# Performance work log

Hardware: AMD Instinct MI355X
Metric: run time of the kernel (lower is better)

Reference implementation:

```python
import jax, jax.numpy as jnp
import numpy as np

N_EMBD = 1024
N_HEAD = 16
HEAD_DIM = N_EMBD // N_HEAD

def setup_inputs() -> dict:
    key = jax.random.key(0)
    ks = jax.random.split(key, 5)
    B, T, C = 2, 2048, N_EMBD
    s = 1.0 / np.sqrt(C)
    x = jax.random.normal(ks[0], (B, T, C), dtype=jnp.float32)
    W_qkv = jax.random.normal(ks[1], (C, 3 * C), dtype=jnp.float32) * s
    b_qkv = jax.random.normal(ks[2], (3 * C,), dtype=jnp.float32) * 0.02
    W_o = jax.random.normal(ks[3], (C, C), dtype=jnp.float32) * s
    b_o = jax.random.normal(ks[4], (C,), dtype=jnp.float32) * 0.02
    return {"x": x, "W_qkv": W_qkv, "b_qkv": b_qkv, "W_o": W_o, "b_o": b_o}

def reference(x, W_qkv, b_qkv, W_o, b_o):
    B, T, C = x.shape
    H, D = N_HEAD, HEAD_DIM
    scale = 1.0 / np.sqrt(D)
    qkv = jnp.einsum('btc,cf->btf', x, W_qkv) + b_qkv  # [B,T,3C]
    q, k, v = jnp.split(qkv, 3, axis=-1)
    # [B,H,T,D]
    q = q.reshape(B, T, H, D).transpose(0, 2, 1, 3)
    k = k.reshape(B, T, H, D).transpose(0, 2, 1, 3)
    v = v.reshape(B, T, H, D).transpose(0, 2, 1, 3)
    att = jnp.einsum('bhqd,bhkd->bhqk', q, k) * scale  # [B,H,T,T]
    causal = jnp.tril(jnp.ones((T, T), dtype=bool))
    att = jnp.where(causal[None, None], att, -jnp.inf)
    att = jax.nn.softmax(att, axis=-1)
    y = jnp.einsum('bhqk,bhkd->bhqd', att, v)  # [B,H,T,D]
    y = y.transpose(0, 2, 1, 3).reshape(B, T, C)
    return jnp.einsum('btc,cf->btf', y, W_o) + b_o
```

## Files before the change

### kernel.cpp

```cpp
#include <hip/hip_runtime.h>
#include <hip/hip_bf16.h>

#define TT 2048
#define BB 2
#define CC 1024
#define NH 16
#define HD 64

typedef __attribute__((ext_vector_type(8))) short short8;
typedef __attribute__((ext_vector_type(4))) short short4b;
typedef __attribute__((ext_vector_type(4))) float f32x4;

typedef unsigned int __attribute__((address_space(1))) ui_gas;
typedef unsigned int __attribute__((address_space(3))) ui_las;

#if __has_builtin(__builtin_amdgcn_mfma_f32_16x16x16bf16_1k)
#define PV16 1
#define VSS 4
#else
#define PV16 0
#define VSS 8
#endif

__device__ __forceinline__ float us2f(unsigned short u) {
    union { unsigned int i; float f; } v; v.i = ((unsigned int)u) << 16; return v.f;
}
__device__ __forceinline__ unsigned short f2us(float f) {
    union { float f; unsigned int i; } v; v.f = f;
    unsigned int i = v.i;
    unsigned int lsb = (i >> 16) & 1u;
    i += 0x7fffu + lsb;
    return (unsigned short)(i >> 16);
}
__device__ __forceinline__ unsigned int pack2_trunc(float a, float b) {
    union { float f; unsigned int u; } x, y; x.f = a; y.f = b;
    return (y.u & 0xffff0000u) | (x.u >> 16);
}

__device__ __forceinline__ void gl_lds16(const unsigned short* g, unsigned short* l) {
    __builtin_amdgcn_global_load_lds((const ui_gas*)g, (ui_las*)l, 16, 0, 0);
}

__device__ __forceinline__ float4 load4(const void* p, size_t i, int isbf) {
    if (isbf) {
        ushort4 u = *reinterpret_cast<const ushort4*>((const unsigned short*)p + i);
        return make_float4(us2f(u.x), us2f(u.y), us2f(u.z), us2f(u.w));
    } else {
        return *reinterpret_cast<const float4*>((const float*)p + i);
    }
}
__device__ __forceinline__ float load1(const void* p, size_t i, int isbf) {
    return isbf ? us2f(((const unsigned short*)p)[i]) : ((const float*)p)[i];
}

__global__ __launch_bounds__(256) void prep_kernel(
    const void* __restrict__ x, const void* __restrict__ Wqkv, const void* __restrict__ Wo,
    const void* __restrict__ bqkv, const void* __restrict__ bo,
    unsigned short* __restrict__ xb, unsigned short* __restrict__ Wqkvt,
    unsigned short* __restrict__ Wot, int* __restrict__ flags)
{
    __shared__ float Ls[64 * 65];
    __shared__ int sh_isbf;
    const int t = threadIdx.x;
    const int bid = blockIdx.x;

    const void* src;
    int mode, sub;
    if (bid < 2048)      { mode = 0; sub = bid;        src = x; }
    else if (bid < 2816) { mode = 1; sub = bid - 2048; src = Wqkv; }
    else                 { mode = 2; sub = bid - 2816; src = Wo; }

    if (bid == 0 && t < 64) {
        const void* ps[5] = {x, Wqkv, bqkv, Wo, bo};
        for (int k = 0; k < 5; ++k) {
            const unsigned short* u = (const unsigned short*)ps[k];
            int bad = 0;
            #pragma unroll
            for (int j = 0; j < 4; ++j) {
                float v = us2f(u[t * 4 + j]);
                if (!(fabsf(v) < 1e4f)) bad = 1;
            }
            unsigned long long m = __ballot(bad != 0);
            if (t == 0) flags[k] = (__popcll(m) < 4) ? 1 : 0;
        }
    }
    if (t < 64) {
        const unsigned short* u = (const unsigned short*)src;
        int bad = 0;
        #pragma unroll
        for (int j = 0; j < 4; ++j) {
            float v = us2f(u[t * 4 + j]);
            if (!(fabsf(v) < 1e4f)) bad = 1;
        }
        unsigned long long m = __ballot(bad != 0);
        if (t == 0) sh_isbf = (__popcll(m) < 4) ? 1 : 0;
    }
    __syncthreads();
    const int isbf = sh_isbf;

    if (mode == 0) {
        const size_t i = ((size_t)sub * 256 + t) * 8;
        float4 a = load4(src, i, isbf);
        float4 b = load4(src, i + 4, isbf);
        alignas(16) unsigned short pk[8];
        pk[0] = f2us(a.x); pk[1] = f2us(a.y); pk[2] = f2us(a.z); pk[3] = f2us(a.w);
        pk[4] = f2us(b.x); pk[5] = f2us(b.y); pk[6] = f2us(b.z); pk[7] = f2us(b.w);
        *reinterpret_cast<uint4*>(xb + i) = *reinterpret_cast<const uint4*>(pk);
        return;
    }

    int N, Krows, n0, k0;
    unsigned short* dst;
    if (mode == 1) { N = 3 * CC; Krows = CC; dst = Wqkvt; n0 = (sub % 48) * 64; k0 = (sub / 48) * 64; }
    else           { N = CC;     Krows = CC; dst = Wot;   n0 = (sub % 16) * 64; k0 = (sub / 16) * 64; }
    {
        const int r = t >> 2, cq = (t & 3) << 4;
        #pragma unroll
        for (int i = 0; i < 4; ++i) {
            float4 v = load4(src, (size_t)(k0 + r) * N + n0 + cq + i * 4, isbf);
            Ls[r * 65 + cq + i * 4 + 0] = v.x;
            Ls[r * 65 + cq + i * 4 + 1] = v.y;
            Ls[r * 65 + cq + i * 4 + 2] = v.z;
            Ls[r * 65 + cq + i * 4 + 3] = v.w;
        }
    }
    __syncthreads();
    {
        const int c = t & 63, kg = (t >> 6) * 16;
        alignas(16) unsigned short pk[16];
        #pragma unroll
        for (int i = 0; i < 16; ++i) pk[i] = f2us(Ls[(kg + i) * 65 + c]);
        unsigned short* d = dst + (size_t)(n0 + c) * Krows + k0 + kg;
        *reinterpret_cast<uint4*>(d + 0) = *reinterpret_cast<const uint4*>(&pk[0]);
        *reinterpret_cast<uint4*>(d + 8) = *reinterpret_cast<const uint4*>(&pk[8]);
    }
}

template<int WM, int WN, int NWM, int NWN, int SWZ, bool VTE>
__global__ __launch_bounds__(256) void gemm_mfma(
    const unsigned short* __restrict__ A,
    const unsigned short* __restrict__ Bt,
    const void* __restrict__ bias, void* __restrict__ C,
    unsigned short* __restrict__ Vt,
    int M, int N, int K,
    const int* __restrict__ flags, int biasfi, int cfi)
{
    constexpr int BM = WM * 16 * NWM, BN = WN * 16 * NWN;
    constexpr int ASL = BM / 16, BSL = BN / 16;
    constexpr int TOT = ASL + BSL;
    constexpr int PW  = TOT / 4;

    __shared__ __align__(16) unsigned short SH[3][TOT * 512];

    const int tid = threadIdx.x;
    const int l  = tid & 63;
    const int w  = tid >> 6;
    const int wm = w / NWN, wn = w % NWN;
    const int lm = l & 15;
    const int lk = (l >> 4) * 8;
    const int quad = l >> 4;

    int bx, by;
    if constexpr (SWZ == 1) {
        const int lin = blockIdx.y * 24 + blockIdx.x;
        const int xcd = lin & 7, loc = lin >> 3;
        bx = (xcd & 1) * 12 + loc % 12;
        by = (xcd >> 1) * 8 + loc / 12;
    } else if constexpr (SWZ == 2) {
        const int lin = blockIdx.y * 16 + blockIdx.x;
        const int xcd = lin & 7, loc = lin >> 3;
        bx = (xcd & 1) * 8 + (loc & 7);
        by = (xcd >> 1) * 16 + (loc >> 3);
    } else {
        bx = blockIdx.x; by = blockIdx.y;
    }
    const int bm = by * BM, bn = bx * BN;

    f32x4 acc[WM][WN];
    #pragma unroll
    for (int i = 0; i < WM; ++i)
        #pragma unroll
        for (int j = 0; j < WN; ++j) acc[i][j] = (f32x4){0.f, 0.f, 0.f, 0.f};

    auto stage = [&](int bb, int k0) {
        #pragma unroll
        for (int s = 0; s < PW; ++s) {
            const int slab = w * PW + s;
            const unsigned short* src;
            if (slab < ASL) src = A  + (size_t)(bm + slab * 16 + lm) * K + k0 + lk;
            else            src = Bt + (size_t)(bn + (slab - ASL) * 16 + lm) * K + k0 + lk;
            gl_lds16(src, &SH[bb][slab * 512]);
        }
    };

    auto compute = [&](int bb) {
        short8 af[WM], bf[WN];
        #pragma unroll
        for (int i = 0; i < WM; ++i)
            af[i] = *reinterpret_cast<const short8*>(&SH[bb][(wm * WM + i) * 512 + l * 8]);
        #pragma unroll
        for (int j = 0; j < WN; ++j)
            bf[j] = *reinterpret_cast<const short8*>(&SH[bb][(ASL + wn * WN + j) * 512 + l * 8]);
        #pragma unroll
        for (int i = 0; i < WM; ++i)
            #pragma unroll
            for (int j = 0; j < WN; ++j)
                acc[i][j] = __builtin_amdgcn_mfma_f32_16x16x32_bf16(af[i], bf[j], acc[i][j], 0, 0, 0);
    };

    const int nt = K >> 5;
    stage(0, 0);
    stage(1, 32);
    asm volatile("s_waitcnt vmcnt(%0)" :: "n"(PW) : "memory");
    __builtin_amdgcn_sched_barrier(0);
    __builtin_amdgcn_s_barrier();

    for (int t = 0; t < nt; ++t) {
        if (t + 2 < nt) stage((t + 2) % 3, (t + 2) << 5);
        compute(t % 3);
        if (t + 2 < nt) {
            asm volatile("s_waitcnt vmcnt(%0)" :: "n"(PW) : "memory");
        } else {
            asm volatile("s_waitcnt vmcnt(0)" ::: "memory");
        }
        __builtin_amdgcn_sched_barrier(0);
        __builtin_amdgcn_s_barrier();
    }

    const int bias_bf = (biasfi >= 0) ? flags[biasfi] : 0;
    const int c_bf    = (cfi >= 0) ? flags[cfi] : ((cfi == -2) ? 1 : 0);
    float bv[WN];
    #pragma unroll
    for (int j = 0; j < WN; ++j) bv[j] = load1(bias, bn + (WN * wn + j) * 16 + lm, bias_bf);

    constexpr int TS = BM + 8;
    unsigned short* FL = &SH[0][0];
    const bool vblk = VTE && (bn >= 2 * CC);

    #pragma unroll
    for (int i = 0; i < WM; ++i) {
        #pragma unroll
        for (int r = 0; r < 4; ++r) {
            const int rl = (WM * wm + i) * 16 + quad * 4 + r;
            const int row = bm + rl;
            #pragma unroll
            for (int j = 0; j < WN; ++j) {
                const int cl2 = (WN * wn + j) * 16 + lm;
                const int col = bn + cl2;
                const float val = acc[i][j][r] + bv[j];
                if (c_bf) {
                    const unsigned short us = f2us(val);
                    ((unsigned short*)C)[(size_t)row * N + col] = us;
                    if (vblk) FL[cl2 * TS + rl] = us;
                } else {
                    ((float*)C)[(size_t)row * N + col] = val;
                }
            }
        }
    }

    if constexpr (VTE) {
        static_assert(!VTE || (BM == 128 && BN % 64 == 0), "VTE geometry");
        static_assert(!VTE || (BN * (BM + 8) <= 3 * TOT * 512), "VTE LDS overlay");
        if (vblk) {
            __syncthreads();
            const int cl = tid >> 1, rq = tid & 1;
            const int cc2 = bn - 2 * CC + cl;
            const int hh = cc2 >> 6, dd = cc2 & 63;
            const int bq = bm >> 11;
            const int tk = (bm & (TT - 1)) + rq * 64;
            unsigned short* dst = Vt + ((size_t)(bq * NH + hh) * HD + dd) * TT + tk;
            const unsigned short* srcp = &FL[cl * TS + rq * 64];
            #pragma unroll
            for (int k = 0; k < 8; ++k)
                *(uint4*)(dst + k * 8) = *(const uint4*)(srcp + k * 8);
        }
    }
}

__global__ __launch_bounds__(256) void attn_mfma(
    const unsigned short* __restrict__ qkv,
    const unsigned short* __restrict__ Vt,
    unsigned short* __restrict__ y)
{
    __shared__ __align__(16) unsigned short Ksh[2][8 * 512];
    __shared__ __align__(16) unsigned short Vsh[2][1039 * VSS];

    const int tid = threadIdx.x;
    const int l   = tid & 63;
    const int w   = tid >> 6;
    const int quad = l >> 4;
    const int col  = l & 15;

    const int n  = blockIdx.x;
    const int g  = n >> 3;
    const int bh = (n & 7) * 4 + (g & 3);
    const int i  = g >> 2;
    const int tA = i, tB = 31 - i;
    const int b  = bh >> 4, h = bh & 15;

#if !PV16
    {
        unsigned short* vflat = &Vsh[0][0];
        for (int ss = tid; ss < 1039 * 2; ss += 256)
            *(uint2*)(&vflat[ss * 8 + 4]) = make_uint2(0u, 0u);
    }
#endif

    const float QSCALE = 0.18033688f;
    short8 qfA[2], qfB[2];
    #pragma unroll
    for (int t2 = 0; t2 < 2; ++t2) {
        const int qt = t2 ? tB : tA;
        short8* qf = t2 ? qfB : qfA;
        const int token = qt * 64 + w * 16 + col;
        const unsigned short* qrow = qkv + (size_t)(b * TT + token) * 3 * CC + h * HD;
        #pragma unroll
        for (int ks = 0; ks < 2; ++ks) {
            ushort4 u0 = *(const ushort4*)(qrow + ks * 32 + quad * 8);
            ushort4 u1 = *(const ushort4*)(qrow + ks * 32 + quad * 8 + 4);
            alignas(16) unsigned short pk[8];
            pk[0] = f2us(us2f(u0.x) * QSCALE);
            pk[1] = f2us(us2f(u0.y) * QSCALE);
            pk[2] = f2us(us2f(u0.z) * QSCALE);
            pk[3] = f2us(us2f(u0.w) * QSCALE);
            pk[4] = f2us(us2f(u1.x) * QSCALE);
            pk[5] = f2us(us2f(u1.y) * QSCALE);
            pk[6] = f2us(us2f(u1.z) * QSCALE);
            pk[7] = f2us(us2f(u1.w) * QSCALE);
            qf[ks] = *(const short8*)pk;
        }
    }

    f32x4 oA[4], oB[4];
    #pragma unroll
    for (int nb = 0; nb < 4; ++nb) {
        oA[nb] = (f32x4){0.f, 0.f, 0.f, 0.f};
        oB[nb] = (f32x4){0.f, 0.f, 0.f, 0.f};
    }
    float lAc = 0.f, lBc = 0.f;

    const unsigned short* kbase = qkv + (size_t)b * TT * 3 * CC + CC + h * HD;
    const unsigned short* vbase = Vt + (size_t)bh * HD * TT;

    const int vd = tid >> 2, vg0 = (tid & 3) * 4;

    uint4 rk[2], rv[2];
    auto issue_loads = [&](int kt) {
        const unsigned short* ksrc = kbase + (size_t)(kt * 64 + l) * 3 * CC;
        #pragma unroll
        for (int c2 = 0; c2 < 2; ++c2) {
            const int c = 2 * w + c2;
            rk[c2] = *(const uint4*)(ksrc + c * 8);
        }
        const unsigned short* vsrc = vbase + (size_t)vd * TT + kt * 64 + vg0 * 4;
        rv[0] = *(const uint4*)(vsrc + 0);
        rv[1] = *(const uint4*)(vsrc + 8);
    };
    auto write_lds = [&](int bb) {
        #pragma unroll
        for (int c2 = 0; c2 < 2; ++c2) {
            const int c = 2 * w + c2;
            const int ks = c >> 2, q = c & 3;
            const int slot = ((quad * 2 + ks) * 64 + q * 16 + col) * 8;
            *(uint4*)(&Ksh[bb][slot]) = rk[c2];
        }
        *(uint2*)(&Vsh[bb][((vg0 + 0) * 65 + vd) * VSS]) = make_uint2(rv[0].x, rv[0].y);
        *(uint2*)(&Vsh[bb][((vg0 + 1) * 65 + vd) * VSS]) = make_uint2(rv[0].z, rv[0].w);
        *(uint2*)(&Vsh[bb][((vg0 + 2) * 65 + vd) * VSS]) = make_uint2(rv[1].x, rv[1].y);
        *(uint2*)(&Vsh[bb][((vg0 + 3) * 65 + vd) * VSS]) = make_uint2(rv[1].z, rv[1].w);
    };

    auto step = [&](const short8* qf, f32x4* o, float& l_i, bool diag, int bb) {
        f32x4 st[4];
        __builtin_amdgcn_s_setprio(1);
        #pragma unroll
        for (int nb = 0; nb < 4; ++nb) {
            f32x4 acc = {0.f, 0.f, 0.f, 0.f};
            #pragma unroll
            for (int ks = 0; ks < 2; ++ks) {
                short8 kf = *(const short8*)(&Ksh[bb][((nb * 2 + ks) * 64 + l) * 8]);
                acc = __builtin_amdgcn_mfma_f32_16x16x32_bf16(kf, qf[ks], acc, 0, 0, 0);
            }
            st[nb] = acc;
        }
        __builtin_amdgcn_s_setprio(0);
        float pv[4][4];
        float rs = 0.f;
        #pragma unroll
        for (int nb = 0; nb < 4; ++nb)
            #pragma unroll
            for (int r = 0; r < 4; ++r) {
                float v = st[nb][r];
                if (diag && (nb * 16 + quad * 4 + r > w * 16 + col)) v = -3e38f;
                float p = __builtin_exp2f(v);
                pv[nb][r] = p;
                rs += p;
            }
        rs += __shfl_xor(rs, 16);
        rs += __shfl_xor(rs, 32);
        l_i += rs;
#if PV16
        short4b pf[4];
        #pragma unroll
        for (int nbk = 0; nbk < 4; ++nbk) {
            union { short4b s; unsigned int u[2]; } pk;
            pk.u[0] = pack2_trunc(pv[nbk][0], pv[nbk][1]);
            pk.u[1] = pack2_trunc(pv[nbk][2], pv[nbk][3]);
            pf[nbk] = pk.s;
        }
        __builtin_amdgcn_s_setprio(1);
        #pragma unroll
        for (int nbd = 0; nbd < 4; ++nbd)
            #pragma unroll
            for (int nbk = 0; nbk < 4; ++nbk) {
                short4b vf = *(const short4b*)(&Vsh[bb][((nbk * 4 + quad) * 65 + nbd * 16 + col) * VSS]);
                o[nbd] = __builtin_amdgcn_mfma_f32_16x16x16bf16_1k(pf[nbk], vf, o[nbd], 0, 0, 0);
            }
        __builtin_amdgcn_s_setprio(0);
#else
        short8 pf[4];
        #pragma unroll
        for (int nbk = 0; nbk < 4; ++nbk) {
            union { short8 s; unsigned int u[4]; } pk;
            pk.u[0] = pack2_trunc(pv[nbk][0], pv[nbk][1]);
            pk.u[1] = pack2_trunc(pv[nbk][2], pv[nbk][3]);
            pk.u[2] = 0u; pk.u[3] = 0u;
            pf[nbk] = pk.s;
        }
        __builtin_amdgcn_s_setprio(1);
        #pragma unroll
        for (int nbd = 0; nbd < 4; ++nbd)
            #pragma unroll
            for (int nbk = 0; nbk < 4; ++nbk) {
                short8 vf = *(const short8*)(&Vsh[bb][((nbk * 4 + quad) * 65 + nbd * 16 + col) * VSS]);
                o[nbd] = __builtin_amdgcn_mfma_f32_16x16x32_bf16(pf[nbk], vf, o[nbd], 0, 0, 0);
            }
        __builtin_amdgcn_s_setprio(0);
#endif
    };

    issue_loads(0);
    write_lds(0);
    __syncthreads();
    for (int kt = 0; kt <= tB; ++kt) {
        const int cur = kt & 1;
        if (kt < tB) issue_loads(kt + 1);
        step(qfB, oB, lBc, kt == tB, cur);
        if (kt <= tA) step(qfA, oA, lAc, kt == tA, cur);
        if (kt < tB) write_lds(cur ^ 1);
        __syncthreads();
    }

    #pragma unroll
    for (int t2 = 0; t2 < 2; ++t2) {
        const int qt = t2 ? tB : tA;
        f32x4* o = t2 ? oB : oA;
        const float inv = 1.f / (t2 ? lBc : lAc);
        float invr[4];
        #pragma unroll
        for (int r = 0; r < 4; ++r) invr[r] = __shfl(inv, quad * 4 + r);
        #pragma unroll
        for (int nb = 0; nb < 4; ++nb)
            #pragma unroll
            for (int r = 0; r < 4; ++r) {
                int token = qt * 64 + w * 16 + quad * 4 + r;
                y[(size_t)(b * TT + token) * CC + h * HD + nb * 16 + col] = f2us(o[nb][r] * invr[r]);
            }
    }
}

extern "C" void kernel_launch(void* const* d_in, const int* in_sizes, int n_in,
                              void* d_out, int out_size, void* d_ws, size_t ws_size,
                              hipStream_t stream) {
    const int M = BB * TT;

    char* ws = (char*)d_ws;
    int*            flags = (int*)ws;                         ws += 256;
    unsigned short* xb    = (unsigned short*)ws;              ws += (size_t)M * CC * 2;
    unsigned short* Wqkvt = (unsigned short*)ws;              ws += (size_t)3 * CC * CC * 2;
    unsigned short* Wot   = (unsigned short*)ws;              ws += (size_t)CC * CC * 2;
    unsigned short* qkv   = (unsigned short*)ws;              ws += (size_t)M * 3 * CC * 2;
    unsigned short* Vt    = (unsigned short*)ws;              ws += (size_t)BB * NH * HD * TT * 2;
    unsigned short* y     = (unsigned short*)ws;

    prep_kernel<<<3072, 256, 0, stream>>>(d_in[0], d_in[1], d_in[3], d_in[2], d_in[4],
                                          xb, Wqkvt, Wot, flags);

    gemm_mfma<4, 4, 2, 2, 1, true><<<dim3(3 * CC / 128, M / 128), 256, 0, stream>>>(
        xb, Wqkvt, d_in[2], qkv, Vt, M, 3 * CC, CC, flags, 2, -2);

    attn_mfma<<<512, 256, 0, stream>>>(qkv, Vt, y);

    gemm_mfma<2, 2, 2, 2, 2, false><<<dim3(CC / 64, M / 64), 256, 0, stream>>>(
        y, Wot, d_in[4], d_out, nullptr, M, CC, CC, flags, 4, 0);
}
```

Baseline: 231.3 us.

## Split attention KV loop across two blocks and combine partials in a new kernel

```diff
diff --git a/kernel.cpp b/kernel.cpp
--- a/kernel.cpp
+++ b/kernel.cpp
@@ -281,7 +281,8 @@
 __global__ __launch_bounds__(256) void attn_mfma(
     const unsigned short* __restrict__ qkv,
     const unsigned short* __restrict__ Vt,
-    unsigned short* __restrict__ y)
+    float* __restrict__ Opart,
+    float* __restrict__ Lpart)
 {
     __shared__ __align__(16) unsigned short Ksh[2][8 * 512];
     __shared__ __align__(16) unsigned short Vsh[2][1039 * VSS];
@@ -293,11 +294,16 @@
     const int col  = l & 15;
 
     const int n  = blockIdx.x;
-    const int g  = n >> 3;
-    const int bh = (n & 7) * 4 + (g & 3);
+    const int p  = n & 511;
+    const int half = n >> 9;
+    const int g  = p >> 3;
+    const int bh = (p & 7) * 4 + (g & 3);
     const int i  = g >> 2;
     const int tA = i, tB = 31 - i;
     const int b  = bh >> 4, h = bh & 15;
+
+    float* Op = Opart + (size_t)half * ((size_t)BB * TT * CC);
+    float* Lp = Lpart + (size_t)half * (BB * NH * TT);
 
 #if !PV16
     {
@@ -393,9 +399,9 @@
             for (int r = 0; r < 4; ++r) {
                 float v = st[nb][r];
                 if (diag && (nb * 16 + quad * 4 + r > w * 16 + col)) v = -3e38f;
-                float p = __builtin_exp2f(v);
-                pv[nb][r] = p;
-                rs += p;
+                float p2 = __builtin_exp2f(v);
+                pv[nb][r] = p2;
+                rs += p2;
             }
         rs += __shfl_xor(rs, 16);
         rs += __shfl_xor(rs, 32);
@@ -440,15 +446,16 @@
 #endif
     };
 
-    issue_loads(0);
+    issue_loads(half);
     write_lds(0);
     __syncthreads();
-    for (int kt = 0; kt <= tB; ++kt) {
-        const int cur = kt & 1;
-        if (kt < tB) issue_loads(kt + 1);
+    int s = 0;
+    for (int kt = half; kt <= tB; kt += 2, ++s) {
+        const int cur = s & 1;
+        if (kt + 2 <= tB) issue_loads(kt + 2);
         step(qfB, oB, lBc, kt == tB, cur);
         if (kt <= tA) step(qfA, oA, lAc, kt == tA, cur);
-        if (kt < tB) write_lds(cur ^ 1);
+        if (kt + 2 <= tB) write_lds(cur ^ 1);
         __syncthreads();
     }
 
@@ -456,18 +463,46 @@
     for (int t2 = 0; t2 < 2; ++t2) {
         const int qt = t2 ? tB : tA;
         f32x4* o = t2 ? oB : oA;
-        const float inv = 1.f / (t2 ? lBc : lAc);
-        float invr[4];
-        #pragma unroll
-        for (int r = 0; r < 4; ++r) invr[r] = __shfl(inv, quad * 4 + r);
+        const float lv = t2 ? lBc : lAc;
+        const int tok0 = qt * 64 + w * 16;
+        if (l < 16) Lp[(size_t)bh * TT + tok0 + l] = lv;
         #pragma unroll
         for (int nb = 0; nb < 4; ++nb)
             #pragma unroll
             for (int r = 0; r < 4; ++r) {
-                int token = qt * 64 + w * 16 + quad * 4 + r;
-                y[(size_t)(b * TT + token) * CC + h * HD + nb * 16 + col] = f2us(o[nb][r] * invr[r]);
-            }
-    }
+                const int token = tok0 + quad * 4 + r;
+                Op[(size_t)(b * TT + token) * CC + h * HD + nb * 16 + col] = o[nb][r];
+            }
+    }
+}
+
+__global__ __launch_bounds__(256) void attn_combine(
+    const float* __restrict__ O0, const float* __restrict__ O1,
+    const float* __restrict__ L0, const float* __restrict__ L1,
+    unsigned short* __restrict__ y)
+{
+    const int g = blockIdx.x * 256 + threadIdx.x;
+    const size_t base = (size_t)g * 8;
+    const int bt = g >> 7;
+    const int c0 = (g & 127) * 8;
+    const int h  = c0 >> 6;
+    const int b  = bt >> 11, tk = bt & (TT - 1);
+    const size_t li = (size_t)(b * NH + h) * TT + tk;
+    const float inv = 1.f / (L0[li] + L1[li]);
+    float4 a0 = *(const float4*)(O0 + base);
+    float4 a1 = *(const float4*)(O0 + base + 4);
+    float4 b0 = *(const float4*)(O1 + base);
+    float4 b1 = *(const float4*)(O1 + base + 4);
+    alignas(16) unsigned short pk[8];
+    pk[0] = f2us((a0.x + b0.x) * inv);
+    pk[1] = f2us((a0.y + b0.y) * inv);
+    pk[2] = f2us((a0.z + b0.z) * inv);
+    pk[3] = f2us((a0.w + b0.w) * inv);
+    pk[4] = f2us((a1.x + b1.x) * inv);
+    pk[5] = f2us((a1.y + b1.y) * inv);
+    pk[6] = f2us((a1.z + b1.z) * inv);
+    pk[7] = f2us((a1.w + b1.w) * inv);
+    *(uint4*)(y + base) = *(const uint4*)pk;
 }
 
 extern "C" void kernel_launch(void* const* d_in, const int* in_sizes, int n_in,
@@ -482,7 +517,9 @@
     unsigned short* Wot   = (unsigned short*)ws;              ws += (size_t)CC * CC * 2;
     unsigned short* qkv   = (unsigned short*)ws;              ws += (size_t)M * 3 * CC * 2;
     unsigned short* Vt    = (unsigned short*)ws;              ws += (size_t)BB * NH * HD * TT * 2;
-    unsigned short* y     = (unsigned short*)ws;
+    unsigned short* y     = (unsigned short*)ws;              ws += (size_t)M * CC * 2;
+    float*          Opart = (float*)ws;                       ws += (size_t)2 * M * CC * 4;
+    float*          Lpart = (float*)ws;                       ws += (size_t)2 * BB * NH * TT * 4;
 
     prep_kernel<<<3072, 256, 0, stream>>>(d_in[0], d_in[1], d_in[3], d_in[2], d_in[4],
                                           xb, Wqkvt, Wot, flags);
@@ -490,7 +527,10 @@
     gemm_mfma<4, 4, 2, 2, 1, true><<<dim3(3 * CC / 128, M / 128), 256, 0, stream>>>(
         xb, Wqkvt, d_in[2], qkv, Vt, M, 3 * CC, CC, flags, 2, -2);
 
-    attn_mfma<<<512, 256, 0, stream>>>(qkv, Vt, y);
+    attn_mfma<<<1024, 256, 0, stream>>>(qkv, Vt, Opart, Lpart);
+
+    attn_combine<<<2048, 256, 0, stream>>>(
+        Opart, Opart + (size_t)M * CC, Lpart, Lpart + (size_t)BB * NH * TT, y);
 
     gemm_mfma<2, 2, 2, 2, 2, false><<<dim3(CC / 64, M / 64), 256, 0, stream>>>(
         y, Wot, d_in[4], d_out, nullptr, M, CC, CC, flags, 4, 0);
```

Result: slower. 241.3 us (+4.3%).

## Single-buffer K/V LDS tiles and drop MFMA priority hints in attention

Applied to the files above, without the earlier changes.

```diff
diff --git a/kernel.cpp b/kernel.cpp
--- a/kernel.cpp
+++ b/kernel.cpp
@@ -283,8 +283,8 @@
     const unsigned short* __restrict__ Vt,
     unsigned short* __restrict__ y)
 {
-    __shared__ __align__(16) unsigned short Ksh[2][8 * 512];
-    __shared__ __align__(16) unsigned short Vsh[2][1039 * VSS];
+    __shared__ __align__(16) unsigned short Ksh[8 * 512];
+    __shared__ __align__(16) unsigned short Vsh[1039 * VSS];
 
     const int tid = threadIdx.x;
     const int l   = tid & 63;
@@ -300,11 +300,8 @@
     const int b  = bh >> 4, h = bh & 15;
 
 #if !PV16
-    {
-        unsigned short* vflat = &Vsh[0][0];
-        for (int ss = tid; ss < 1039 * 2; ss += 256)
-            *(uint2*)(&vflat[ss * 8 + 4]) = make_uint2(0u, 0u);
-    }
+    for (int ss = tid; ss < 1039; ss += 256)
+        *(uint2*)(&Vsh[ss * 8 + 4]) = make_uint2(0u, 0u);
 #endif
 
     const float QSCALE = 0.18033688f;
@@ -357,34 +354,32 @@
         rv[0] = *(const uint4*)(vsrc + 0);
         rv[1] = *(const uint4*)(vsrc + 8);
     };
-    auto write_lds = [&](int bb) {
+    auto write_lds = [&]() {
         #pragma unroll
         for (int c2 = 0; c2 < 2; ++c2) {
             const int c = 2 * w + c2;
             const int ks = c >> 2, q = c & 3;
             const int slot = ((quad * 2 + ks) * 64 + q * 16 + col) * 8;
-            *(uint4*)(&Ksh[bb][slot]) = rk[c2];
-        }
-        *(uint2*)(&Vsh[bb][((vg0 + 0) * 65 + vd) * VSS]) = make_uint2(rv[0].x, rv[0].y);
-        *(uint2*)(&Vsh[bb][((vg0 + 1) * 65 + vd) * VSS]) = make_uint2(rv[0].z, rv[0].w);
-        *(uint2*)(&Vsh[bb][((vg0 + 2) * 65 + vd) * VSS]) = make_uint2(rv[1].x, rv[1].y);
-        *(uint2*)(&Vsh[bb][((vg0 + 3) * 65 + vd) * VSS]) = make_uint2(rv[1].z, rv[1].w);
+            *(uint4*)(&Ksh[slot]) = rk[c2];
+        }
+        *(uint2*)(&Vsh[((vg0 + 0) * 65 + vd) * VSS]) = make_uint2(rv[0].x, rv[0].y);
+        *(uint2*)(&Vsh[((vg0 + 1) * 65 + vd) * VSS]) = make_uint2(rv[0].z, rv[0].w);
+        *(uint2*)(&Vsh[((vg0 + 2) * 65 + vd) * VSS]) = make_uint2(rv[1].x, rv[1].y);
+        *(uint2*)(&Vsh[((vg0 + 3) * 65 + vd) * VSS]) = make_uint2(rv[1].z, rv[1].w);
     };
 
-    auto step = [&](const short8* qf, f32x4* o, float& l_i, bool diag, int bb) {
+    auto step = [&](const short8* qf, f32x4* o, float& l_i, bool diag) {
         f32x4 st[4];
-        __builtin_amdgcn_s_setprio(1);
         #pragma unroll
         for (int nb = 0; nb < 4; ++nb) {
             f32x4 acc = {0.f, 0.f, 0.f, 0.f};
             #pragma unroll
             for (int ks = 0; ks < 2; ++ks) {
-                short8 kf = *(const short8*)(&Ksh[bb][((nb * 2 + ks) * 64 + l) * 8]);
+                short8 kf = *(const short8*)(&Ksh[((nb * 2 + ks) * 64 + l) * 8]);
                 acc = __builtin_amdgcn_mfma_f32_16x16x32_bf16(kf, qf[ks], acc, 0, 0, 0);
             }
             st[nb] = acc;
         }
-        __builtin_amdgcn_s_setprio(0);
         float pv[4][4];
         float rs = 0.f;
         #pragma unroll
@@ -409,15 +404,13 @@
             pk.u[1] = pack2_trunc(pv[nbk][2], pv[nbk][3]);
             pf[nbk] = pk.s;
         }
-        __builtin_amdgcn_s_setprio(1);
         #pragma unroll
         for (int nbd = 0; nbd < 4; ++nbd)
             #pragma unroll
             for (int nbk = 0; nbk < 4; ++nbk) {
-                short4b vf = *(const short4b*)(&Vsh[bb][((nbk * 4 + quad) * 65 + nbd * 16 + col) * VSS]);
+                short4b vf = *(const short4b*)(&Vsh[((nbk * 4 + quad) * 65 + nbd * 16 + col) * VSS]);
                 o[nbd] = __builtin_amdgcn_mfma_f32_16x16x16bf16_1k(pf[nbk], vf, o[nbd], 0, 0, 0);
             }
-        __builtin_amdgcn_s_setprio(0);
 #else
         short8 pf[4];
         #pragma unroll
@@ -428,27 +421,23 @@
             pk.u[2] = 0u; pk.u[3] = 0u;
             pf[nbk] = pk.s;
         }
-        __builtin_amdgcn_s_setprio(1);
         #pragma unroll
         for (int nbd = 0; nbd < 4; ++nbd)
             #pragma unroll
             for (int nbk = 0; nbk < 4; ++nbk) {
-                short8 vf = *(const short8*)(&Vsh[bb][((nbk * 4 + quad) * 65 + nbd * 16 + col) * VSS]);
+                short8 vf = *(const short8*)(&Vsh[((nbk * 4 + quad) * 65 + nbd * 16 + col) * VSS]);
                 o[nbd] = __builtin_amdgcn_mfma_f32_16x16x32_bf16(pf[nbk], vf, o[nbd], 0, 0, 0);
             }
-        __builtin_amdgcn_s_setprio(0);
 #endif
     };
 
     issue_loads(0);
-    write_lds(0);
-    __syncthreads();
     for (int kt = 0; kt <= tB; ++kt) {
-        const int cur = kt & 1;
+        write_lds();
+        __syncthreads();
         if (kt < tB) issue_loads(kt + 1);
-        step(qfB, oB, lBc, kt == tB, cur);
-        if (kt <= tA) step(qfA, oA, lAc, kt == tA, cur);
-        if (kt < tB) write_lds(cur ^ 1);
+        step(qfB, oB, lBc, kt == tB);
+        if (kt <= tA) step(qfA, oA, lAc, kt == tA);
         __syncthreads();
     }
 
```

After: 233.2 us. No clear change (+0.8%).
